# Performance work log

Hardware: AMD Instinct MI355X
Metric: run time of the kernel (lower is better)

Reference implementation:

```python
import jax, jax.numpy as jnp
import numpy as np


def _rank_transform_ascending(flat):
    # torch: _, idx = sort(flat, descending=False); flat[idx] = linspace(0,1,n)+1/n
    n = flat.shape[0]
    order = jnp.argsort(flat)  # ascending
    prob = jnp.linspace(0.0, 1.0, n, dtype=flat.dtype) + jnp.asarray(1.0 / n, flat.dtype)
    return jnp.zeros_like(flat).at[order].set(prob)


def corr_attention(query, key, value):
    # score[b,h,i,j] = cosine-like similarity q_i . k_j / (|q_i| |k_j|)
    score = jnp.einsum('bhid,bhjd->bhij', query, key)
    q_len = jnp.sqrt(jnp.sum(query * query, axis=-1, keepdims=True)) + 1e-5  # [b,h,s,1]
    k_len = jnp.sqrt(jnp.sum(key * key, axis=-1, keepdims=True)) + 1e-5      # [b,h,s,1]
    score = score / (q_len * jnp.swapaxes(k_len, -1, -2))
    signal = jnp.sign(score)
    size = score.shape
    flat = jnp.abs(score).reshape(-1)
    ranked = _rank_transform_ascending(flat)
    score = -jnp.log(ranked).reshape(size) * signal
    score = score / jnp.sum(jnp.abs(score), axis=-1, keepdims=True)
    return jnp.einsum('bhij,bhjd->bhid', score, value)


def setup_inputs() -> dict:
    key0 = jax.random.key(0)
    kq, kk, kv = jax.random.split(key0, 3)
    B, H, S, D = 4, 8, 1024, 64
    query = jax.random.normal(kq, (B, H, S, D), dtype=jnp.float32)
    key = jax.random.normal(kk, (B, H, S, D), dtype=jnp.float32)
    value = jax.random.normal(kv, (B, H, S, D), dtype=jnp.float32)
    return {"query": query, "key": key, "value": value}


def reference(query, key, value):
    # Attention.forward with mode='season'
    return corr_attention(query, key, value)
```

## Files before the change

kernel.cpp:

```cpp
#include <hip/hip_runtime.h>
#include <math.h>
#include <stdint.h>

#define S_LEN 1024
#define D_DIM 64
#define BH    32
#define KSHIFT 13
#define NBINS 130048u
#define CODE_BASE 97280u
#define NB2   32768u
#define HIST_LO_C 20480u
#define NHOT_H  12288u
#define NCHUNK 64
#define HBLK   256
#define INV_NM1 (1.0f/33554431.0f)
#define INV_N   (2.9802322387695312e-08f)
#define FIX_TH  1e-4f


typedef _Float16 half8 __attribute__((ext_vector_type(8)));
typedef short    short8 __attribute__((ext_vector_type(8)));
typedef float    floatx4 __attribute__((ext_vector_type(4)));

__device__ __forceinline__ void bf16_split(float x, short& hi, short& lo) {
  unsigned u = __float_as_uint(x);
  unsigned h = (u + 0x7FFFu + ((u >> 16) & 1u)) >> 16;
  float hf = __uint_as_float(h << 16);
  float lf = x - hf;
  hi = (short)h;
  lo = (short)(__float_as_uint(lf) >> 16);
}

__global__ __launch_bounds__(256) void norms_kernel(
    const float* __restrict__ Q, const float* __restrict__ K,
    double* __restrict__ qinvD, double* __restrict__ kinvD,
    unsigned short* __restrict__ Qhi_g, unsigned short* __restrict__ Qlo_g,
    unsigned short* __restrict__ Khi_g, unsigned short* __restrict__ Klo_g) {
  int row  = blockIdx.x * 4 + (threadIdx.x >> 6);
  int lane = threadIdx.x & 63;
  const float* src; double* dstD; unsigned short *hD, *lD; int r = row;
  if (row < BH * S_LEN) { src = Q; dstD = qinvD; hD = Qhi_g; lD = Qlo_g; }
  else { src = K; dstD = kinvD; hD = Khi_g; lD = Klo_g; r = row - BH * S_LEN; }
  float xf = src[(size_t)r * D_DIM + lane];
  double v = (double)xf;
  double s = v * v;
  #pragma unroll
  for (int off = 32; off; off >>= 1) s += __shfl_down(s, off);
  double inv = 0.0;
  if (lane == 0) {
    inv = 1.0 / (sqrt(s) + 1e-5);
    dstD[r] = inv;
  }
  inv = __shfl(inv, 0);
  float x = xf * (float)inv;
  short hi, lo;
  bf16_split(x, hi, lo);
  hD[(size_t)r * D_DIM + lane] = (unsigned short)hi;
  lD[(size_t)r * D_DIM + lane] = (unsigned short)lo;
}

__global__ __launch_bounds__(256) void qk_mfma_kernel(
    const float* __restrict__ Q, const float* __restrict__ K,
    const unsigned short* __restrict__ Qhi_g, const unsigned short* __restrict__ Qlo_g,
    const unsigned short* __restrict__ Khi_g, const unsigned short* __restrict__ Klo_g,
    const double* __restrict__ qinvD, const double* __restrict__ kinvD,
    unsigned short* __restrict__ code16) {
  __shared__ short Qhi[64][72], Qlo[64][72];
  __shared__ short Khi[64][72], Klo[64][72];
  int bh = blockIdx.z;
  int i0 = blockIdx.y * 64;
  int j0 = blockIdx.x * 64;
  int tid = threadIdx.x;
  {
    const unsigned short* Qh = Qhi_g + ((size_t)bh * S_LEN + i0) * D_DIM;
    const unsigned short* Ql = Qlo_g + ((size_t)bh * S_LEN + i0) * D_DIM;
    const unsigned short* Kh = Khi_g + ((size_t)bh * S_LEN + j0) * D_DIM;
    const unsigned short* Kl = Klo_g + ((size_t)bh * S_LEN + j0) * D_DIM;
    #pragma unroll
    for (int l = 0; l < 2; ++l) {
      int idx = l * 256 + tid;
      int row = idx >> 3, c = (idx & 7) * 8;
      *(uint4*)&Qhi[row][c] = *(const uint4*)(Qh + (size_t)row * D_DIM + c);
      *(uint4*)&Qlo[row][c] = *(const uint4*)(Ql + (size_t)row * D_DIM + c);
      *(uint4*)&Khi[row][c] = *(const uint4*)(Kh + (size_t)row * D_DIM + c);
      *(uint4*)&Klo[row][c] = *(const uint4*)(Kl + (size_t)row * D_DIM + c);
    }
  }
  __syncthreads();
  int wave = tid >> 6;
  int lane = tid & 63;
  int m    = lane & 15;
  int quad = lane >> 4;
  floatx4 acc[4];
  #pragma unroll
  for (int n = 0; n < 4; ++n) acc[n] = (floatx4){0.f, 0.f, 0.f, 0.f};
  #pragma unroll
  for (int ks = 0; ks < 2; ++ks) {
    int kb = ks * 32 + quad * 8;
    short8 a_hi = *(const short8*)&Qhi[wave * 16 + m][kb];
    short8 a_lo = *(const short8*)&Qlo[wave * 16 + m][kb];
    #pragma unroll
    for (int nt = 0; nt < 4; ++nt) {
      short8 b_hi = *(const short8*)&Khi[nt * 16 + m][kb];
      short8 b_lo = *(const short8*)&Klo[nt * 16 + m][kb];
      acc[nt] = __builtin_amdgcn_mfma_f32_16x16x32_bf16(a_hi, b_hi, acc[nt], 0, 0, 0);
      acc[nt] = __builtin_amdgcn_mfma_f32_16x16x32_bf16(a_hi, b_lo, acc[nt], 0, 0, 0);
      acc[nt] = __builtin_amdgcn_mfma_f32_16x16x32_bf16(a_lo, b_hi, acc[nt], 0, 0, 0);
    }
  }
  #pragma unroll
  for (int nt = 0; nt < 4; ++nt) {
    #pragma unroll
    for (int r = 0; r < 4; ++r) {
      unsigned long long am = __ballot(fabsf(acc[nt][r]) < FIX_TH);
      while (am) {
        int src = (int)(__ffsll((long long)am) - 1);
        am &= am - 1;
        int i_s = i0 + wave * 16 + (src >> 4) * 4 + r;
        int j_s = j0 + nt * 16 + (src & 15);
        double qd = (double)Q[((size_t)bh * S_LEN + i_s) * D_DIM + lane];
        double kd = (double)K[((size_t)bh * S_LEN + j_s) * D_DIM + lane];
        double pd = qd * kd;
        #pragma unroll
        for (int off = 32; off; off >>= 1) pd += __shfl_down(pd, off);
        float corr = 0.f;
        if (lane == 0)
          corr = (float)(pd * qinvD[(size_t)bh * S_LEN + i_s] * kinvD[(size_t)bh * S_LEN + j_s]);
        corr = __shfl(corr, 0);
        if (lane == src) acc[nt][r] = corr;
      }
    }
  }
  #pragma unroll
  for (int r = 0; r < 4; ++r) {
    unsigned short* op = code16 + (size_t)bh * 1048576 + (size_t)(j0 >> 6) * 65536
                       + (size_t)(i0 + wave * 16 + quad * 4 + r) * 64 + m;
    #pragma unroll
    for (int nt = 0; nt < 4; ++nt) {
      unsigned u = __float_as_uint(acc[nt][r]);
      unsigned a = u & 0x7fffffffu;
      unsigned b = a >> KSHIFT;
      if (b > NBINS - 1u) b = NBINS - 1u;
      unsigned c = (b < CODE_BASE) ? 0u : (b - CODE_BASE);
      op[nt * 16] = (unsigned short)(c | ((u >> 16) & 0x8000u));
    }
  }
}

__global__ __launch_bounds__(1024) void hist_kernel(
    const uint4* __restrict__ codes, unsigned* __restrict__ hist,
    unsigned char* __restrict__ partial) {
  __shared__ unsigned lh[NHOT_H];
  int tid = threadIdx.x;
  for (unsigned i = tid; i < NHOT_H; i += 1024) lh[i] = 0u;
  __syncthreads();
  const uint4* p = codes + (size_t)blockIdx.x * 16384;
  #pragma unroll 2
  for (int it = 0; it < 16; ++it) {
    uint4 w = p[it * 1024 + tid];
    unsigned ws[4] = {w.x, w.y, w.z, w.w};
    #pragma unroll
    for (int k = 0; k < 4; ++k) {
      unsigned c0 = ws[k] & 0x7fffu;
      unsigned c1 = (ws[k] >> 16) & 0x7fffu;
      if (c0 >= HIST_LO_C) atomicAdd(&lh[c0 - HIST_LO_C], 1u);
      else                 atomicAdd(&hist[c0], 1u);
      if (c1 >= HIST_LO_C) atomicAdd(&lh[c1 - HIST_LO_C], 1u);
      else                 atomicAdd(&hist[c1], 1u);
    }
  }
  __syncthreads();
  unsigned char* dst = partial + (size_t)blockIdx.x * NHOT_H;
  for (unsigned i = tid; i < NHOT_H; i += 1024) dst[i] = (unsigned char)lh[i];
}

__global__ __launch_bounds__(256) void hreduce_kernel(
    const unsigned char* __restrict__ partial, unsigned* __restrict__ hist) {
  unsigned bin = blockIdx.x * 256 + threadIdx.x;
  unsigned s = 0;
  #pragma unroll 8
  for (int b = 0; b < HBLK; ++b) s += (unsigned)partial[(size_t)b * NHOT_H + bin];
  hist[HIST_LO_C + bin] = s;
}

__global__ __launch_bounds__(256) void vt_kernel(
    const float* __restrict__ V, _Float16* __restrict__ Vt) {
  __shared__ _Float16 T[64][72];
  int bh = blockIdx.y, j0 = blockIdx.x * 64, tid = threadIdx.x;
  const float* Vb = V + ((size_t)bh * S_LEN + j0) * D_DIM;
  #pragma unroll
  for (int l = 0; l < 4; ++l) {
    int idx = l * 256 + tid;
    int jr = idx >> 4, d4 = idx & 15;
    float4 v = ((const float4*)Vb)[idx];
    T[d4*4+0][jr] = (_Float16)v.x;
    T[d4*4+1][jr] = (_Float16)v.y;
    T[d4*4+2][jr] = (_Float16)v.z;
    T[d4*4+3][jr] = (_Float16)v.w;
  }
  __syncthreads();
  _Float16* Ob = Vt + (size_t)(bh * 16 + blockIdx.x) * 4096;
  #pragma unroll
  for (int l = 0; l < 2; ++l) {
    int idx = l * 256 + tid;
    int d = idx >> 3, jc = idx & 7;
    uint4 val = *(const uint4*)&T[d][jc*8];
    *(uint4*)(Ob + (size_t)d * 64 + jc*8) = val;
  }
}

__global__ __launch_bounds__(256) void scan1_kernel(const unsigned* __restrict__ hist,
                                                    unsigned* __restrict__ csum) {
  __shared__ unsigned sd[256];
  int c = blockIdx.x, t = threadIdx.x;
  const unsigned* p = hist + (size_t)c * 512;
  sd[t] = p[t] + p[t + 256];
  __syncthreads();
  for (int off = 128; off; off >>= 1) {
    if (t < off) sd[t] += sd[t + off];
    __syncthreads();
  }
  if (t == 0) csum[c] = sd[0];
}

__global__ __launch_bounds__(256) void scan2_kernel(unsigned* __restrict__ csum) {
  __shared__ unsigned d[256];
  int t = threadIdx.x;
  unsigned v = (t < NCHUNK) ? csum[t] : 0u;
  d[t] = v; __syncthreads();
  for (int off = 1; off < 256; off <<= 1) {
    unsigned x = (t >= off) ? d[t - off] : 0u;
    __syncthreads();
    d[t] += x;
    __syncthreads();
  }
  if (t < NCHUNK) csum[t] = d[t] - v;
}

__global__ __launch_bounds__(256) void scan3_kernel(const unsigned* __restrict__ hist,
                                                    const unsigned* __restrict__ csum,
                                                    _Float16* __restrict__ tab2) {
  __shared__ unsigned ts[256];
  int c = blockIdx.x, t = threadIdx.x;
  const unsigned* p = hist + (size_t)c * 512 + t * 2;
  unsigned l0 = p[0], l1 = p[1];
  unsigned s = l0 + l1;
  ts[t] = s; __syncthreads();
  for (int off = 1; off < 256; off <<= 1) {
    unsigned x = (t >= off) ? ts[t - off] : 0u;
    __syncthreads();
    ts[t] += x;
    __syncthreads();
  }
  unsigned base = csum[c] + ts[t] - s;
  int idx = c * 512 + t * 2;
  float r0 = (float)base + 0.5f * ((float)l0 - 1.0f);
  tab2[idx]     = (_Float16)(-__logf(fmaf(r0, INV_NM1, INV_N)));
  float r1 = (float)(base + l0) + 0.5f * ((float)l1 - 1.0f);
  tab2[idx + 1] = (_Float16)(-__logf(fmaf(r1, INV_NM1, INV_N)));
}

__global__ __launch_bounds__(256) void pv_mfma_kernel(
    const unsigned short* __restrict__ code16, const _Float16* __restrict__ Vt,
    const unsigned short* __restrict__ tab2, float* __restrict__ out) {
  __shared__ unsigned short ldsT[NB2];
  int tid = threadIdx.x;
  {
    const uint4* gsrc = (const uint4*)tab2;
    uint4* ldst = (uint4*)ldsT;
    #pragma unroll
    for (int i = 0; i < 16; ++i)
      ldst[i * 256 + tid] = gsrc[i * 256 + tid];
  }
  __syncthreads();

  int bh   = blockIdx.y;
  int wave = tid >> 6;
  int lane = tid & 63;
  int m    = lane & 15;
  int quad = lane >> 4;
  int i0   = blockIdx.x * 64 + wave * 16;
  const unsigned short* Sb = code16 + (size_t)bh * 1048576 + (size_t)(i0 + m) * 64;
  const _Float16*       Vb = Vt + (size_t)bh * 65536;

  floatx4 acc[4];
  #pragma unroll
  for (int n = 0; n < 4; ++n) acc[n] = (floatx4){0.f, 0.f, 0.f, 0.f};
  float rsum = 0.f;

  uint4 cwA, cwB;
  {
    int ka = 0 * 32 + quad * 8;
    cwA = *(const uint4*)(Sb + (size_t)(ka >> 6) * 65536 + (ka & 63));
    int kb = 1 * 32 + quad * 8;
    cwB = *(const uint4*)(Sb + (size_t)(kb >> 6) * 65536 + (kb & 63));
  }
  #pragma unroll
  for (int ks = 0; ks < 32; ++ks) {
    uint4 cur = (ks & 1) ? cwB : cwA;
    if (ks + 2 < 32) {
      int kp = (ks + 2) * 32 + quad * 8;
      uint4 nx = *(const uint4*)(Sb + (size_t)(kp >> 6) * 65536 + (kp & 63));
      if (ks & 1) cwB = nx; else cwA = nx;
    }
    int k0  = ks * 32 + quad * 8;
    int jt  = k0 >> 6;
    int jin = k0 & 63;
    unsigned ww[4] = {cur.x, cur.y, cur.z, cur.w};
    union { unsigned short u[8]; half8 h; } af;
    #pragma unroll
    for (int e = 0; e < 8; ++e) {
      unsigned cd = (e & 1) ? (ww[e >> 1] >> 16) : (ww[e >> 1] & 0xffffu);
      unsigned short tb = ldsT[cd & 0x7fffu];
      af.u[e] = (unsigned short)(tb ^ (cd & 0x8000u));
      unsigned short tabs = (unsigned short)(tb & 0x7fffu);
      rsum += (float)__builtin_bit_cast(_Float16, tabs);
    }
    half8 bf[4];
    #pragma unroll
    for (int n = 0; n < 4; ++n)
      bf[n] = *(const half8*)(Vb + (size_t)jt * 4096 + (size_t)(n * 16 + m) * 64 + jin);
    #pragma unroll
    for (int n = 0; n < 4; ++n)
      acc[n] = __builtin_amdgcn_mfma_f32_16x16x32_f16(af.h, bf[n], acc[n], 0, 0, 0);
  }

  rsum += __shfl_xor(rsum, 16);
  rsum += __shfl_xor(rsum, 32);
  float inv = 1.0f / rsum;
  #pragma unroll
  for (int r = 0; r < 4; ++r) {
    int row = quad * 4 + r;
    float invr = __shfl(inv, row);
    float* op = out + ((size_t)bh * S_LEN + i0 + row) * D_DIM + m;
    #pragma unroll
    for (int n = 0; n < 4; ++n)
      op[n * 16] = acc[n][r] * invr;
  }
}

extern "C" void kernel_launch(void* const* d_in, const int* in_sizes, int n_in,
                              void* d_out, int out_size, void* d_ws, size_t ws_size,
                              hipStream_t stream) {
  const float* Q = (const float*)d_in[0];
  const float* K = (const float*)d_in[1];
  const float* V = (const float*)d_in[2];
  float* out = (float*)d_out;
  char* ws = (char*)d_ws;
  unsigned short* code16  = (unsigned short*)(ws);
  unsigned*       hist    = (unsigned*)(ws + 67108864);
  unsigned char*  partial = (unsigned char*)(ws + 67239936);
  double*         qinvD   = (double*)(ws + 67239936 + 3145728);
  double*         kinvD   = (double*)(ws + 67239936 + 3407872);
  _Float16*       Vt      = (_Float16*)(ws + 67239936);
  unsigned*       csum    = (unsigned*)(ws + 67239936 + 4194304);
  _Float16*       tab2    = (_Float16*)(ws + 67239936 + 4195328);
  unsigned short* Qhi_g   = (unsigned short*)(ws + 71503872);
  unsigned short* Qlo_g   = (unsigned short*)(ws + 75698176);
  unsigned short* Khi_g   = (unsigned short*)(ws + 79892480);
  unsigned short* Klo_g   = (unsigned short*)(ws + 84086784);

  hipMemsetAsync(hist, 0, NB2 * sizeof(unsigned), stream);
  norms_kernel<<<(2 * BH * S_LEN) / 4, 256, 0, stream>>>(
      Q, K, qinvD, kinvD, Qhi_g, Qlo_g, Khi_g, Klo_g);
  qk_mfma_kernel<<<dim3(16, 16, BH), 256, 0, stream>>>(
      Q, K, Qhi_g, Qlo_g, Khi_g, Klo_g, qinvD, kinvD, code16);
  hist_kernel<<<HBLK, 1024, 0, stream>>>((const uint4*)code16, hist, partial);
  hreduce_kernel<<<NHOT_H / 256, 256, 0, stream>>>(partial, hist);
  vt_kernel<<<dim3(16, BH), 256, 0, stream>>>(V, Vt);
  scan1_kernel<<<NCHUNK, 256, 0, stream>>>(hist, csum);
  scan2_kernel<<<1, 256, 0, stream>>>(csum);
  scan3_kernel<<<NCHUNK, 256, 0, stream>>>(hist, csum, tab2);
  pv_mfma_kernel<<<dim3(16, BH), 256, 0, stream>>>(
      code16, Vt, (const unsigned short*)tab2, out);
}
```

Baseline: 203.3 us.

## Stage V tiles in padded LDS and double the PV block to 512 threads

The PV kernel now runs 8 waves per block covering 128 rows, which halves how many times the 64KB rank table is copied into LDS across the grid. V tiles for each 256-column chunk are staged into padded LDS, so the waves share them instead of each reading V from global memory. Score codes for the next chunk are prefetched eight loads at a time. In exchange the grid shrinks to 256 blocks, and with LDS use at about 100KB there is roughly one block per CU. Two barriers per chunk are added and overlap across blocks is reduced.

```diff
diff --git a/kernel.cpp b/kernel.cpp
--- a/kernel.cpp
+++ b/kernel.cpp
@@ -260,69 +260,97 @@
   tab2[idx + 1] = (_Float16)(-__logf(fmaf(r1, INV_NM1, INV_N)));
 }
 
-__global__ __launch_bounds__(256) void pv_mfma_kernel(
+__global__ __launch_bounds__(512, 1) void pv_mfma_kernel(
     const unsigned short* __restrict__ code16, const _Float16* __restrict__ Vt,
     const unsigned short* __restrict__ tab2, float* __restrict__ out) {
   __shared__ unsigned short ldsT[NB2];
+  __shared__ _Float16 vlds[4 * 64 * 72];
   int tid = threadIdx.x;
-  {
-    const uint4* gsrc = (const uint4*)tab2;
-    uint4* ldst = (uint4*)ldsT;
-    #pragma unroll
-    for (int i = 0; i < 16; ++i)
-      ldst[i * 256 + tid] = gsrc[i * 256 + tid];
-  }
-  __syncthreads();
 
   int bh   = blockIdx.y;
   int wave = tid >> 6;
   int lane = tid & 63;
   int m    = lane & 15;
   int quad = lane >> 4;
-  int i0   = blockIdx.x * 64 + wave * 16;
+  int i0   = blockIdx.x * 128 + wave * 16;
   const unsigned short* Sb = code16 + (size_t)bh * 1048576 + (size_t)(i0 + m) * 64;
   const _Float16*       Vb = Vt + (size_t)bh * 65536;
 
+  {
+    const uint4* gsrc = (const uint4*)tab2;
+    uint4* ldst = (uint4*)ldsT;
+    #pragma unroll
+    for (int i = 0; i < 8; ++i)
+      ldst[i * 512 + tid] = gsrc[i * 512 + tid];
+  }
+  #pragma unroll
+  for (int it = 0; it < 4; ++it) {
+    int u = it * 512 + tid;
+    int e0 = u * 8;
+    int tt = e0 >> 12, rem = e0 & 4095, d = rem >> 6, jin = rem & 63;
+    uint4 val = *(const uint4*)(Vb + 0 * 16384 + e0);
+    *(uint4*)&vlds[tt * 4608 + d * 72 + jin] = val;
+  }
+  uint4 cw[8];
+  #pragma unroll
+  for (int s = 0; s < 8; ++s) {
+    int k0 = 0 * 256 + s * 32 + quad * 8;
+    cw[s] = *(const uint4*)(Sb + (size_t)(k0 >> 6) * 65536 + (k0 & 63));
+  }
+  __syncthreads();
+
   floatx4 acc[4];
   #pragma unroll
   for (int n = 0; n < 4; ++n) acc[n] = (floatx4){0.f, 0.f, 0.f, 0.f};
   float rsum = 0.f;
 
-  uint4 cwA, cwB;
-  {
-    int ka = 0 * 32 + quad * 8;
-    cwA = *(const uint4*)(Sb + (size_t)(ka >> 6) * 65536 + (ka & 63));
-    int kb = 1 * 32 + quad * 8;
-    cwB = *(const uint4*)(Sb + (size_t)(kb >> 6) * 65536 + (kb & 63));
-  }
-  #pragma unroll
-  for (int ks = 0; ks < 32; ++ks) {
-    uint4 cur = (ks & 1) ? cwB : cwA;
-    if (ks + 2 < 32) {
-      int kp = (ks + 2) * 32 + quad * 8;
-      uint4 nx = *(const uint4*)(Sb + (size_t)(kp >> 6) * 65536 + (kp & 63));
-      if (ks & 1) cwB = nx; else cwA = nx;
-    }
-    int k0  = ks * 32 + quad * 8;
-    int jt  = k0 >> 6;
-    int jin = k0 & 63;
-    unsigned ww[4] = {cur.x, cur.y, cur.z, cur.w};
-    union { unsigned short u[8]; half8 h; } af;
-    #pragma unroll
-    for (int e = 0; e < 8; ++e) {
-      unsigned cd = (e & 1) ? (ww[e >> 1] >> 16) : (ww[e >> 1] & 0xffffu);
-      unsigned short tb = ldsT[cd & 0x7fffu];
-      af.u[e] = (unsigned short)(tb ^ (cd & 0x8000u));
-      unsigned short tabs = (unsigned short)(tb & 0x7fffu);
-      rsum += (float)__builtin_bit_cast(_Float16, tabs);
-    }
-    half8 bf[4];
-    #pragma unroll
-    for (int n = 0; n < 4; ++n)
-      bf[n] = *(const half8*)(Vb + (size_t)jt * 4096 + (size_t)(n * 16 + m) * 64 + jin);
-    #pragma unroll
-    for (int n = 0; n < 4; ++n)
-      acc[n] = __builtin_amdgcn_mfma_f32_16x16x32_f16(af.h, bf[n], acc[n], 0, 0, 0);
+  #pragma unroll
+  for (int c = 0; c < 4; ++c) {
+    uint4 cwn[8];
+    if (c < 3) {
+      #pragma unroll
+      for (int s = 0; s < 8; ++s) {
+        int k0 = (c + 1) * 256 + s * 32 + quad * 8;
+        cwn[s] = *(const uint4*)(Sb + (size_t)(k0 >> 6) * 65536 + (k0 & 63));
+      }
+    }
+    #pragma unroll
+    for (int s = 0; s < 8; ++s) {
+      int lk  = s * 32 + quad * 8;
+      int tt  = lk >> 6;
+      int jin = lk & 63;
+      unsigned ww[4] = {cw[s].x, cw[s].y, cw[s].z, cw[s].w};
+      union { unsigned short u[8]; half8 h; } af;
+      #pragma unroll
+      for (int e = 0; e < 8; ++e) {
+        unsigned cd = (e & 1) ? (ww[e >> 1] >> 16) : (ww[e >> 1] & 0xffffu);
+        unsigned short tb = ldsT[cd & 0x7fffu];
+        af.u[e] = (unsigned short)(tb ^ (cd & 0x8000u));
+        unsigned short tabs = (unsigned short)(tb & 0x7fffu);
+        rsum += (float)__builtin_bit_cast(_Float16, tabs);
+      }
+      half8 bf[4];
+      #pragma unroll
+      for (int n = 0; n < 4; ++n)
+        bf[n] = *(const half8*)&vlds[tt * 4608 + (n * 16 + m) * 72 + jin];
+      #pragma unroll
+      for (int n = 0; n < 4; ++n)
+        acc[n] = __builtin_amdgcn_mfma_f32_16x16x32_f16(af.h, bf[n], acc[n], 0, 0, 0);
+    }
+    if (c < 3) {
+      __syncthreads();
+      #pragma unroll
+      for (int it = 0; it < 4; ++it) {
+        int u = it * 512 + tid;
+        int e0 = u * 8;
+        int tt = e0 >> 12, rem = e0 & 4095, d = rem >> 6, jin = rem & 63;
+        uint4 val = *(const uint4*)(Vb + (size_t)(c + 1) * 16384 + e0);
+        *(uint4*)&vlds[tt * 4608 + d * 72 + jin] = val;
+      }
+      __syncthreads();
+      #pragma unroll
+      for (int s = 0; s < 8; ++s) cw[s] = cwn[s];
+    }
   }
 
   rsum += __shfl_xor(rsum, 16);
@@ -371,6 +399,6 @@
   scan1_kernel<<<NCHUNK, 256, 0, stream>>>(hist, csum);
   scan2_kernel<<<1, 256, 0, stream>>>(csum);
   scan3_kernel<<<NCHUNK, 256, 0, stream>>>(hist, csum, tab2);
-  pv_mfma_kernel<<<dim3(16, BH), 256, 0, stream>>>(
+  pv_mfma_kernel<<<dim3(8, BH), 512, 0, stream>>>(
       code16, Vt, (const unsigned short*)tab2, out);
 }
```

Measured after the change: 191.1 us. -6.0%, faster.
